# Optimization experiments

Measured on AMD Instinct MI355X. Metric: run time of the kernel, lower is better.

Reference implementation:

```python
import jax, jax.numpy as jnp
import numpy as np

B, CIN, COUT, H, W = 4, 256, 256, 64, 64
DG, K, PAD = 4, 3, 1  # deformable groups, kernel size, padding
KK = K * K


def setup_inputs() -> dict:
    key = jax.random.key(0)
    k1, k2, k3, k4 = jax.random.split(key, 4)
    x = jax.random.normal(k1, (B, CIN, H, W), jnp.float32)
    shape = jax.random.normal(k2, (B, 2, H, W), jnp.float32)
    # conv_offset: Conv2d(2, DG*2*K*K, 3, pad=1, bias=False), init std=0.1
    w_offset = jax.random.normal(k3, (DG * 2 * KK, 2, K, K), jnp.float32) * 0.1
    # deform conv weight: [COUT, CIN, K, K], init std=0.01
    w_deform = jax.random.normal(k4, (COUT, CIN, K, K), jnp.float32) * 0.01
    return {"x": x, "shape": shape, "w_offset": w_offset, "w_deform": w_deform}


def _conv2d(x, w, pad):
    return jax.lax.conv_general_dilated(
        x, w, window_strides=(1, 1), padding=[(pad, pad), (pad, pad)],
        dimension_numbers=("NCHW", "OIHW", "NCHW"))


def _deform_conv(x, offset, w):
    """DCN v1 (mmcv DeformConv, stride=1, dilation=1, groups=1)."""
    Bn, C, Hh, Ww = x.shape
    Cg = C // DG
    # offset channel layout: [DG, KK, (dy, dx)]
    off = offset.reshape(Bn, DG, KK, 2, Hh, Ww)
    dy, dx = off[:, :, :, 0], off[:, :, :, 1]          # [B, DG, KK, H, W]
    ky, kx = jnp.meshgrid(jnp.arange(K), jnp.arange(K), indexing="ij")
    # base sampling grid: p0 + pn  (stride 1, pad PAD)
    grid_y = ky.reshape(KK, 1, 1) + jnp.arange(Hh).reshape(1, Hh, 1) - PAD  # [KK,H,1]
    grid_x = kx.reshape(KK, 1, 1) + jnp.arange(Ww).reshape(1, 1, Ww) - PAD  # [KK,1,W]
    sy = dy + grid_y[None, None].astype(dy.dtype)       # [B, DG, KK, H, W]
    sx = dx + grid_x[None, None].astype(dx.dtype)

    y0 = jnp.floor(sy)
    x0 = jnp.floor(sx)
    ly = (sy - y0).reshape(Bn, DG, 1, -1)               # [B, DG, 1, KK*H*W]
    lx = (sx - x0).reshape(Bn, DG, 1, -1)
    y0i = y0.astype(jnp.int32)
    x0i = x0.astype(jnp.int32)

    xg = x.reshape(Bn, DG, Cg, Hh * Ww)                 # per-group channels

    def corner(yi, xi):
        valid = (yi >= 0) & (yi <= Hh - 1) & (xi >= 0) & (xi <= Ww - 1)
        yc = jnp.clip(yi, 0, Hh - 1)
        xc = jnp.clip(xi, 0, Ww - 1)
        idx = (yc * Ww + xc).reshape(Bn, DG, -1)        # [B, DG, KK*H*W]
        v = jnp.take_along_axis(xg, idx[:, :, None, :], axis=3)  # [B,DG,Cg,KK*H*W]
        return v * valid.reshape(Bn, DG, 1, -1).astype(v.dtype)

    v00 = corner(y0i, x0i)
    v01 = corner(y0i, x0i + 1)
    v10 = corner(y0i + 1, x0i)
    v11 = corner(y0i + 1, x0i + 1)
    val = (v00 * (1 - ly) * (1 - lx) + v01 * (1 - ly) * lx
           + v10 * ly * (1 - lx) + v11 * ly * lx)       # [B, DG, Cg, KK*H*W]

    # im2col columns -> GEMM with weight
    cols = val.reshape(Bn, C * KK, Hh * Ww)
    out = jnp.einsum("oc,bcp->bop", w.reshape(w.shape[0], C * KK), cols)
    return out.reshape(Bn, w.shape[0], Hh, Ww)


def reference(x, shape, w_offset, w_deform):
    offset = _conv2d(shape, w_offset, PAD)              # [B, DG*2*KK, H, W]
    return jax.nn.relu(_deform_conv(x, offset, w_deform))
```

## Files before the change

kernel.cpp:

```cpp
#include <hip/hip_runtime.h>
#include <hip/hip_bf16.h>
#include <stdint.h>

typedef __attribute__((ext_vector_type(8))) short bf16x8;
typedef __attribute__((ext_vector_type(4))) float f32x4;
typedef __attribute__((ext_vector_type(4))) unsigned int u32x4;

__device__ __forceinline__ float u2f(unsigned int u) {
  union { unsigned int i; float f; } c; c.i = u; return c.f;
}
__device__ __forceinline__ unsigned int f2b(float f) {
  union { float f; unsigned int i; } c; c.f = f;
  unsigned int x = c.i;
  return (x + 0x7fffu + ((x >> 16) & 1u)) >> 16;
}

__global__ __launch_bounds__(256) void k_prep(
    const float* __restrict__ shape, const float* __restrict__ w_off,
    const float* __restrict__ x, const float* __restrict__ wd,
    char* __restrict__ desc, unsigned short* __restrict__ xt,
    unsigned short* __restrict__ wp) {
  __shared__ float tile[64][65];
  int bid = blockIdx.x;
  int t = threadIdx.x;
  if (bid < 576) {
    int band = bid & 3;
    int rem = bid >> 2;
    int b = rem / 36, r2 = rem % 36, g = r2 / 9, kk = r2 % 9;
    int ky = kk / 3, kx = kk - ky * 3;
    int ocy = g * 18 + kk * 2;
    float wy[18], wx[18];
#pragma unroll
    for (int i = 0; i < 18; ++i) { wy[i] = w_off[ocy * 18 + i]; wx[i] = w_off[(ocy + 1) * 18 + i]; }
    const float* sp = shape + (size_t)b * 2 * 4096;
    char* dp = desc + (size_t)rem * 4096 * 16;
#pragma unroll
    for (int e = 0; e < 4; ++e) {
      int p = band * 1024 + t * 4 + e;
      int y = p >> 6, xx0 = p & 63;
      float dy = 0.f, dx = 0.f;
#pragma unroll
      for (int ic = 0; ic < 2; ++ic)
#pragma unroll
        for (int kyy = 0; kyy < 3; ++kyy) {
          int yy = y + kyy - 1;
          if (yy < 0 || yy > 63) continue;
#pragma unroll
          for (int kxx = 0; kxx < 3; ++kxx) {
            int xx = xx0 + kxx - 1;
            if (xx < 0 || xx > 63) continue;
            float sv = sp[ic * 4096 + yy * 64 + xx];
            dy += sv * wy[ic * 9 + kyy * 3 + kxx];
            dx += sv * wx[ic * 9 + kyy * 3 + kxx];
          }
        }
      float sy = dy + (float)(y + ky - 1);
      float sx = dx + (float)(xx0 + kx - 1);
      float fy = floorf(sy), fx = floorf(sx);
      float ly = sy - fy, lx = sx - fx;
      int y0 = (int)fy, x0 = (int)fx;
      float vy0 = (y0 >= 0 && y0 <= 63) ? 1.f : 0.f;
      float vy1 = (y0 >= -1 && y0 <= 62) ? 1.f : 0.f;
      float vx0 = (x0 >= 0 && x0 <= 63) ? 1.f : 0.f;
      float vx1 = (x0 >= -1 && x0 <= 62) ? 1.f : 0.f;
      float w00 = (1.f - ly) * (1.f - lx) * vy0 * vx0;
      float w01 = (1.f - ly) * lx * vy0 * vx1;
      float w10 = ly * (1.f - lx) * vy1 * vx0;
      float w11 = ly * lx * vy1 * vx1;
      unsigned int yc0 = (unsigned int)min(max(y0, 0), 63);
      unsigned int yc1 = (unsigned int)min(max(y0 + 1, 0), 63);
      unsigned int xc0 = (unsigned int)min(max(x0, 0), 63);
      unsigned int xc1 = (unsigned int)min(max(x0 + 1, 0), 63);
      u32x4 d;
      d[0] = (yc0 * 64 + xc0) | ((yc0 * 64 + xc1) << 16);
      d[1] = (yc1 * 64 + xc0) | ((yc1 * 64 + xc1) << 16);
      d[2] = f2b(w00) | (f2b(w01) << 16);
      d[3] = f2b(w10) | (f2b(w11) << 16);
      *(u32x4*)(dp + (size_t)p * 16) = d;
    }
  } else if (bid < 1600) {
    int id = bid - 576;
    int b = id >> 8, ct = (id >> 6) & 3, pt = id & 63;
    int c0 = ct * 64, p0 = pt * 64;
#pragma unroll
    for (int i = 0; i < 4; ++i) {
      int row = (t >> 4) + i * 16;
      int seg = t & 15;
      float4 v = *(const float4*)&x[(size_t)(b * 256 + c0 + row) * 4096 + p0 + seg * 4];
      tile[row][seg * 4 + 0] = v.x;
      tile[row][seg * 4 + 1] = v.y;
      tile[row][seg * 4 + 2] = v.z;
      tile[row][seg * 4 + 3] = v.w;
    }
    __syncthreads();
    {
      int pl = t >> 2;
      int cs = (t & 3) * 16;
      unsigned int wbuf[8];
#pragma unroll
      for (int j = 0; j < 8; ++j)
        wbuf[j] = f2b(tile[cs + 2 * j][pl]) | (f2b(tile[cs + 2 * j + 1][pl]) << 16);
      unsigned short* dst = xt + (size_t)(b * 4096 + p0 + pl) * 256 + c0 + cs;
      *(u32x4*)(dst) = *(u32x4*)&wbuf[0];
      *(u32x4*)(dst + 8) = *(u32x4*)&wbuf[4];
    }
  } else {
    int id = (bid - 1600) * 256 + t;
    int m = id >> 8, ci = id & 255;
    int g = ci >> 6, c = ci & 63;
    int cs = c ^ ((m & 7) << 3);
    const float* src = wd + (size_t)(m * 256 + ci) * 9;
    float v[9];
#pragma unroll
    for (int kk = 0; kk < 9; ++kk) v[kk] = src[kk];
#pragma unroll
    for (int kk = 0; kk < 9; ++kk)
      wp[(size_t)(kk * 4 + g) * 16384 + m * 64 + cs] = (unsigned short)f2b(v[kk]);
  }
}

struct CSet { uint2 v0, v1, v2, v3; unsigned int w01, w23; };

#define DESC_LD(c, dv) do { \
    dv = *(const u32x4*)(descb + (size_t)(((c) & 3) * 9 + ((c) >> 2)) * 65536); \
  } while (0)

#define CORNERS(S, dv, cc) do { \
    unsigned int base_ = (unsigned int)(((cc) & 3) << 7) + cb8; \
    (S).v0 = *(const uint2*)(xtbB + (((dv)[0] & 0xffffu) << 9) + base_); \
    (S).v1 = *(const uint2*)(xtbB + (((dv)[0] >> 16) << 9) + base_); \
    (S).v2 = *(const uint2*)(xtbB + (((dv)[1] & 0xffffu) << 9) + base_); \
    (S).v3 = *(const uint2*)(xtbB + (((dv)[1] >> 16) << 9) + base_); \
    (S).w01 = (dv)[2]; \
    (S).w23 = (dv)[3]; \
  } while (0)

#define BLEND(S, bbuf) do { \
    float w0_ = u2f((S).w01 << 16), w1_ = u2f((S).w01 & 0xffff0000u); \
    float w2_ = u2f((S).w23 << 16), w3_ = u2f((S).w23 & 0xffff0000u); \
    uint2 o_; \
    { \
      float lo_ = w0_ * u2f((S).v0.x << 16) + w1_ * u2f((S).v1.x << 16) \
                + w2_ * u2f((S).v2.x << 16) + w3_ * u2f((S).v3.x << 16); \
      float hi_ = w0_ * u2f((S).v0.x & 0xffff0000u) + w1_ * u2f((S).v1.x & 0xffff0000u) \
                + w2_ * u2f((S).v2.x & 0xffff0000u) + w3_ * u2f((S).v3.x & 0xffff0000u); \
      o_.x = f2b(lo_) | (f2b(hi_) << 16); \
    } \
    { \
      float lo_ = w0_ * u2f((S).v0.y << 16) + w1_ * u2f((S).v1.y << 16) \
                + w2_ * u2f((S).v2.y << 16) + w3_ * u2f((S).v3.y << 16); \
      float hi_ = w0_ * u2f((S).v0.y & 0xffff0000u) + w1_ * u2f((S).v1.y & 0xffff0000u) \
                + w2_ * u2f((S).v2.y & 0xffff0000u) + w3_ * u2f((S).v3.y & 0xffff0000u); \
      o_.y = f2b(lo_) | (f2b(hi_) << 16); \
    } \
    *(uint2*)((bbuf) + bwr) = o_; \
  } while (0)

#define STAGE_A(c, abuf) do { \
    const unsigned short* asrc_ = wp + (size_t)(c) * 16384 + t * 8; \
    _Pragma("unroll") for (int i_ = 0; i_ < 4; ++i_) \
      __builtin_amdgcn_global_load_lds( \
          (const __attribute__((address_space(1))) unsigned int*)(asrc_ + i_ * 4096), \
          (__attribute__((address_space(3))) unsigned int*)((abuf) + t * 16 + i_ * 8192), \
          16, 0, 0); \
  } while (0)

#define MFMA_STEP(abuf, bbuf) do { \
    _Pragma("unroll") for (int ks_ = 0; ks_ < 2; ++ks_) { \
      int kb_ = ks_ * 64 + kq; \
      bf16x8 a0_ = *(const bf16x8*)((abuf) + (wid * 32 + lm) * 128 + (kb_ ^ swz)); \
      bf16x8 a1_ = *(const bf16x8*)((abuf) + (wid * 32 + 16 + lm) * 128 + (kb_ ^ swz)); \
      bf16x8 b0_ = *(const bf16x8*)((bbuf) + lm * 128 + (kb_ ^ swz)); \
      bf16x8 b1_ = *(const bf16x8*)((bbuf) + (16 + lm) * 128 + (kb_ ^ swz)); \
      acc00 = __builtin_amdgcn_mfma_f32_16x16x32_bf16(a0_, b0_, acc00, 0, 0, 0); \
      acc01 = __builtin_amdgcn_mfma_f32_16x16x32_bf16(a0_, b1_, acc01, 0, 0, 0); \
      acc10 = __builtin_amdgcn_mfma_f32_16x16x32_bf16(a1_, b0_, acc10, 0, 0, 0); \
      acc11 = __builtin_amdgcn_mfma_f32_16x16x32_bf16(a1_, b1_, acc11, 0, 0, 0); \
    } \
  } while (0)

#define PHASE(c, Acur, Anext, Bcur, Bnext, Sfill, Sblend, dvUse, dvFill) do { \
    { int ca_ = (c) + 1 < 36 ? (c) + 1 : 35; STAGE_A(ca_, Anext); } \
    { int cc_ = (c) + 2 < 36 ? (c) + 2 : 35; CORNERS(Sfill, dvUse, cc_); } \
    { int cd_ = (c) + 3 < 36 ? (c) + 3 : 35; DESC_LD(cd_, dvFill); } \
    MFMA_STEP(Acur, Bcur); \
    BLEND(Sblend, Bnext); \
    asm volatile("s_waitcnt lgkmcnt(0)" ::: "memory"); \
    asm volatile("s_waitcnt vmcnt(5)" ::: "memory"); \
    __builtin_amdgcn_s_barrier(); \
  } while (0)

__global__ __launch_bounds__(512, 4) void k_deform_main(
    const unsigned short* __restrict__ xt, const unsigned short* __restrict__ wp,
    const char* __restrict__ desc, float* __restrict__ out) {
  __shared__ __align__(16) char lds[73728];
  const int t = threadIdx.x;
  const int l = t & 63;
  const int wid = t >> 6;

  int orig = blockIdx.x;
  int bid = (orig & 7) * 64 + (orig >> 3);
  const int xh = bid & 1;
  const int rowid = bid >> 1;
  const int b = rowid >> 6;
  const int y = rowid & 63;

  const int p = t >> 4;
  const int cq = t & 15;
  const unsigned int cb8 = cq * 8;
  const int bwr = p * 128 + ((cq * 8) ^ ((p & 7) << 4));

  const int lm = l & 15;
  const int kq = (l >> 4) << 4;
  const int swz = (lm & 7) << 4;

  f32x4 acc00 = {}, acc01 = {}, acc10 = {}, acc11 = {};

  const char* descb = desc + (size_t)(b * 36 * 4096 + y * 64 + xh * 32 + p) * 16;
  const char* xtbB = (const char*)(xt + (size_t)b * 4096 * 256);

  char* ldsA0 = lds;
  char* ldsA1 = lds + 32768;
  char* ldsB0 = lds + 65536;
  char* ldsB1 = lds + 69632;

  CSet SE, SO;
  u32x4 dvA, dvB;

  {
    u32x4 d0, d1;
    DESC_LD(0, d0);
    DESC_LD(1, d1);
    DESC_LD(2, dvA);
    STAGE_A(0, ldsA0);
    CSet St;
    CORNERS(St, d0, 0);
    BLEND(St, ldsB0);
    CORNERS(SO, d1, 1);
    asm volatile("s_waitcnt lgkmcnt(0)" ::: "memory");
    asm volatile("s_waitcnt vmcnt(4)" ::: "memory");
    __builtin_amdgcn_s_barrier();
  }

  for (int pr = 0; pr < 18; ++pr) {
    const int c = pr * 2;
    PHASE(c,     ldsA0, ldsA1, ldsB0, ldsB1, SE, SO, dvA, dvB);
    PHASE(c + 1, ldsA1, ldsA0, ldsB1, ldsB0, SO, SE, dvB, dvA);
  }

  const int lm4 = (l >> 4) << 2;
  float* ob = out + (size_t)(b * 256 + wid * 32) * 4096 + y * 64 + xh * 32;
#pragma unroll
  for (int r = 0; r < 4; ++r) {
    ob[(size_t)(lm4 + r) * 4096 + lm] = fmaxf(acc00[r], 0.f);
    ob[(size_t)(lm4 + r) * 4096 + 16 + lm] = fmaxf(acc01[r], 0.f);
    ob[(size_t)(16 + lm4 + r) * 4096 + lm] = fmaxf(acc10[r], 0.f);
    ob[(size_t)(16 + lm4 + r) * 4096 + 16 + lm] = fmaxf(acc11[r], 0.f);
  }
}

extern "C" void kernel_launch(void* const* d_in, const int* in_sizes, int n_in,
                              void* d_out, int out_size, void* d_ws, size_t ws_size,
                              hipStream_t stream) {
  const float* x     = (const float*)d_in[0];
  const float* shape = (const float*)d_in[1];
  const float* w_off = (const float*)d_in[2];
  const float* w_def = (const float*)d_in[3];
  float* out = (float*)d_out;
  char* ws = (char*)d_ws;

  char* desc          = ws;
  unsigned short* xt  = (unsigned short*)(ws + 9437184);
  unsigned short* wpk = (unsigned short*)(ws + 9437184 + 8388608);

  k_prep<<<1856, 256, 0, stream>>>(shape, w_off, x, w_def, desc, xt, wpk);
  k_deform_main<<<512, 512, 0, stream>>>(xt, wpk, desc, out);
}
```

Before: 69.94 us.

## Single-buffer weight tiles in LDS and raise occupancy target

Drops the double-buffered A (weight) tile so the LDS footprint shrinks from 72 KB to 40 KB, and raises the launch-bounds occupancy hint from 4 to 8. Each phase now runs the MFMA step first, then waits on a barrier before overwriting the single A buffer with the next chunk. Corner gathers and the blend for the next B tile still overlap with that load. The goal is more resident blocks per CU to hide gather latency. The cost is an extra barrier per phase, less overlap between weight staging and MFMA, and a tighter register budget that may cause spills. With only 512 blocks in the grid, higher occupancy may not be reachable anyway.

```diff
diff --git a/kernel.cpp b/kernel.cpp
--- a/kernel.cpp
+++ b/kernel.cpp
@@ -156,20 +156,20 @@
     *(uint2*)((bbuf) + bwr) = o_; \
   } while (0)
 
-#define STAGE_A(c, abuf) do { \
+#define STAGE_A(c) do { \
     const unsigned short* asrc_ = wp + (size_t)(c) * 16384 + t * 8; \
     _Pragma("unroll") for (int i_ = 0; i_ < 4; ++i_) \
       __builtin_amdgcn_global_load_lds( \
           (const __attribute__((address_space(1))) unsigned int*)(asrc_ + i_ * 4096), \
-          (__attribute__((address_space(3))) unsigned int*)((abuf) + t * 16 + i_ * 8192), \
+          (__attribute__((address_space(3))) unsigned int*)(ldsA + t * 16 + i_ * 8192), \
           16, 0, 0); \
   } while (0)
 
-#define MFMA_STEP(abuf, bbuf) do { \
+#define MFMA_STEP(bbuf) do { \
     _Pragma("unroll") for (int ks_ = 0; ks_ < 2; ++ks_) { \
       int kb_ = ks_ * 64 + kq; \
-      bf16x8 a0_ = *(const bf16x8*)((abuf) + (wid * 32 + lm) * 128 + (kb_ ^ swz)); \
-      bf16x8 a1_ = *(const bf16x8*)((abuf) + (wid * 32 + 16 + lm) * 128 + (kb_ ^ swz)); \
+      bf16x8 a0_ = *(const bf16x8*)(ldsA + (wid * 32 + lm) * 128 + (kb_ ^ swz)); \
+      bf16x8 a1_ = *(const bf16x8*)(ldsA + (wid * 32 + 16 + lm) * 128 + (kb_ ^ swz)); \
       bf16x8 b0_ = *(const bf16x8*)((bbuf) + lm * 128 + (kb_ ^ swz)); \
       bf16x8 b1_ = *(const bf16x8*)((bbuf) + (16 + lm) * 128 + (kb_ ^ swz)); \
       acc00 = __builtin_amdgcn_mfma_f32_16x16x32_bf16(a0_, b0_, acc00, 0, 0, 0); \
@@ -179,21 +179,23 @@
     } \
   } while (0)
 
-#define PHASE(c, Acur, Anext, Bcur, Bnext, Sfill, Sblend, dvUse, dvFill) do { \
-    { int ca_ = (c) + 1 < 36 ? (c) + 1 : 35; STAGE_A(ca_, Anext); } \
-    { int cc_ = (c) + 2 < 36 ? (c) + 2 : 35; CORNERS(Sfill, dvUse, cc_); } \
-    { int cd_ = (c) + 3 < 36 ? (c) + 3 : 35; DESC_LD(cd_, dvFill); } \
-    MFMA_STEP(Acur, Bcur); \
-    BLEND(Sblend, Bnext); \
+#define PHASE(c, Bcur, Bnext, Scur, Snext, dvU, dvF) do { \
+    MFMA_STEP(Bcur); \
+    asm volatile("s_waitcnt lgkmcnt(0)" ::: "memory"); \
+    __builtin_amdgcn_s_barrier(); \
+    { int ca_ = (c) + 1 < 36 ? (c) + 1 : 35; STAGE_A(ca_); } \
+    { int cc_ = (c) + 2 < 36 ? (c) + 2 : 35; CORNERS(Snext, dvU, cc_); } \
+    { int cd_ = (c) + 3 < 36 ? (c) + 3 : 35; DESC_LD(cd_, dvF); } \
+    BLEND(Scur, Bnext); \
     asm volatile("s_waitcnt lgkmcnt(0)" ::: "memory"); \
     asm volatile("s_waitcnt vmcnt(5)" ::: "memory"); \
     __builtin_amdgcn_s_barrier(); \
   } while (0)
 
-__global__ __launch_bounds__(512, 4) void k_deform_main(
+__global__ __launch_bounds__(512, 8) void k_deform_main(
     const unsigned short* __restrict__ xt, const unsigned short* __restrict__ wp,
     const char* __restrict__ desc, float* __restrict__ out) {
-  __shared__ __align__(16) char lds[73728];
+  __shared__ __align__(16) char lds[40960];
   const int t = threadIdx.x;
   const int l = t & 63;
   const int wid = t >> 6;
@@ -219,10 +221,9 @@
   const char* descb = desc + (size_t)(b * 36 * 4096 + y * 64 + xh * 32 + p) * 16;
   const char* xtbB = (const char*)(xt + (size_t)b * 4096 * 256);
 
-  char* ldsA0 = lds;
-  char* ldsA1 = lds + 32768;
-  char* ldsB0 = lds + 65536;
-  char* ldsB1 = lds + 69632;
+  char* ldsA = lds;
+  char* ldsB0 = lds + 32768;
+  char* ldsB1 = lds + 36864;
 
   CSet SE, SO;
   u32x4 dvA, dvB;
@@ -232,11 +233,11 @@
     DESC_LD(0, d0);
     DESC_LD(1, d1);
     DESC_LD(2, dvA);
-    STAGE_A(0, ldsA0);
+    STAGE_A(0);
     CSet St;
     CORNERS(St, d0, 0);
     BLEND(St, ldsB0);
-    CORNERS(SO, d1, 1);
+    CORNERS(SE, d1, 1);
     asm volatile("s_waitcnt lgkmcnt(0)" ::: "memory");
     asm volatile("s_waitcnt vmcnt(4)" ::: "memory");
     __builtin_amdgcn_s_barrier();
@@ -244,8 +245,8 @@
 
   for (int pr = 0; pr < 18; ++pr) {
     const int c = pr * 2;
-    PHASE(c,     ldsA0, ldsA1, ldsB0, ldsB1, SE, SO, dvA, dvB);
-    PHASE(c + 1, ldsA1, ldsA0, ldsB1, ldsB0, SO, SE, dvB, dvA);
+    PHASE(c,     ldsB0, ldsB1, SE, SO, dvA, dvB);
+    PHASE(c + 1, ldsB1, ldsB0, SO, SE, dvB, dvA);
   }
 
   const int lm4 = (l >> 4) << 2;
```

Result: slower. 94.43 us (+35.0%).

## Process two K-chunks per barrier phase with deeper prefetch pipeline

Applied to the files above, without the earlier changes.

Restructures the main loop so each phase runs MFMA on both double-buffered chunks, then stages the next two A chunks, gathers corners for two chunks further ahead, and loads descriptors six to seven chunks ahead. The number of barrier phases per row drops from 36 to 18 and global gather latency gets more time to hide. In exchange it needs twice as many live corner sets and descriptor registers, which may hurt occupancy or cause spills under launch_bounds(512,4). Each phase now also has two barriers, with staging and MFMA serialized rather than interleaved.

```diff
diff --git a/kernel.cpp b/kernel.cpp
--- a/kernel.cpp
+++ b/kernel.cpp
@@ -179,14 +179,21 @@
     } \
   } while (0)
 
-#define PHASE(c, Acur, Anext, Bcur, Bnext, Sfill, Sblend, dvUse, dvFill) do { \
-    { int ca_ = (c) + 1 < 36 ? (c) + 1 : 35; STAGE_A(ca_, Anext); } \
-    { int cc_ = (c) + 2 < 36 ? (c) + 2 : 35; CORNERS(Sfill, dvUse, cc_); } \
-    { int cd_ = (c) + 3 < 36 ? (c) + 3 : 35; DESC_LD(cd_, dvFill); } \
-    MFMA_STEP(Acur, Bcur); \
-    BLEND(Sblend, Bnext); \
+#define PHASE2(c, Sre, Sro, Sfe, Sfo, dvUe, dvUo, dvFe, dvFo) do { \
+    MFMA_STEP(ldsA0, ldsB0); \
+    MFMA_STEP(ldsA1, ldsB1); \
     asm volatile("s_waitcnt lgkmcnt(0)" ::: "memory"); \
-    asm volatile("s_waitcnt vmcnt(5)" ::: "memory"); \
+    __builtin_amdgcn_s_barrier(); \
+    { int c2_ = (c) + 2 < 36 ? (c) + 2 : 35; STAGE_A(c2_, ldsA0); } \
+    { int c3_ = (c) + 3 < 36 ? (c) + 3 : 35; STAGE_A(c3_, ldsA1); } \
+    { int c4_ = (c) + 4 < 36 ? (c) + 4 : 35; CORNERS(Sfe, dvUe, c4_); } \
+    { int c5_ = (c) + 5 < 36 ? (c) + 5 : 35; CORNERS(Sfo, dvUo, c5_); } \
+    { int c6_ = (c) + 6 < 36 ? (c) + 6 : 35; DESC_LD(c6_, dvFe); } \
+    { int c7_ = (c) + 7 < 36 ? (c) + 7 : 35; DESC_LD(c7_, dvFo); } \
+    BLEND(Sre, ldsB0); \
+    BLEND(Sro, ldsB1); \
+    asm volatile("s_waitcnt lgkmcnt(0)" ::: "memory"); \
+    asm volatile("s_waitcnt vmcnt(10)" ::: "memory"); \
     __builtin_amdgcn_s_barrier(); \
   } while (0)
 
@@ -224,28 +231,34 @@
   char* ldsB0 = lds + 65536;
   char* ldsB1 = lds + 69632;
 
-  CSet SE, SO;
-  u32x4 dvA, dvB;
+  CSet S0e, S0o, S1e, S1o;
+  u32x4 dvAe, dvAo, dvBe, dvBo;
 
   {
-    u32x4 d0, d1;
+    u32x4 d0, d1, d2, d3;
     DESC_LD(0, d0);
     DESC_LD(1, d1);
-    DESC_LD(2, dvA);
+    DESC_LD(2, d2);
+    DESC_LD(3, d3);
     STAGE_A(0, ldsA0);
-    CSet St;
-    CORNERS(St, d0, 0);
-    BLEND(St, ldsB0);
-    CORNERS(SO, d1, 1);
+    STAGE_A(1, ldsA1);
+    CSet St0, St1;
+    CORNERS(St0, d0, 0);
+    CORNERS(St1, d1, 1);
+    BLEND(St0, ldsB0);
+    BLEND(St1, ldsB1);
+    CORNERS(S0e, d2, 2);
+    CORNERS(S0o, d3, 3);
+    DESC_LD(4, dvAe);
+    DESC_LD(5, dvAo);
     asm volatile("s_waitcnt lgkmcnt(0)" ::: "memory");
-    asm volatile("s_waitcnt vmcnt(4)" ::: "memory");
     __builtin_amdgcn_s_barrier();
   }
 
-  for (int pr = 0; pr < 18; ++pr) {
-    const int c = pr * 2;
-    PHASE(c,     ldsA0, ldsA1, ldsB0, ldsB1, SE, SO, dvA, dvB);
-    PHASE(c + 1, ldsA1, ldsA0, ldsB1, ldsB0, SO, SE, dvB, dvA);
+  for (int pr = 0; pr < 9; ++pr) {
+    const int c = pr * 4;
+    PHASE2(c,     S0e, S0o, S1e, S1o, dvAe, dvAo, dvBe, dvBo);
+    PHASE2(c + 2, S1e, S1o, S0e, S0o, dvBe, dvBo, dvAe, dvAo);
   }
 
   const int lm4 = (l >> 4) << 2;
```

Result: slower. 73.59 us (+5.2%).
